# Kernel tuning notes

Hardware: AMD Instinct MI355X
Metric: run time of the kernel (lower is better)

Reference implementation:

```python
import jax, jax.numpy as jnp
import numpy as np

EPS = 1e-12  # matches tf l2_normalize epsilon behavior closely enough for testing

def setup_inputs() -> dict:
    key = jax.random.key(0)
    k1, k2 = jax.random.split(key)
    B, M, D = 512, 65536, 512
    context = jax.random.normal(k1, (B, D), dtype=jnp.float32)
    memory = jax.random.normal(k2, (M, D), dtype=jnp.float32)
    return {"context": context, "memory": memory}

def reference(context, memory):
    # tf.keras.losses.cosine_similarity returns NEGATIVE cosine similarity:
    # sim[b,m] = -sum(l2norm(context[b]) * l2norm(memory[m]))
    ctx_n = context / jnp.sqrt(jnp.maximum(jnp.sum(context * context, axis=-1, keepdims=True), EPS))
    mem_n = memory / jnp.sqrt(jnp.maximum(jnp.sum(memory * memory, axis=-1, keepdims=True), EPS))
    sim = -jnp.einsum('bd,md->bm', ctx_n, mem_n)  # [B, M]
    best = jnp.argmin(sim, axis=-1)               # [B], = argmax cosine
    # recall: gather then expand_dims(axis=0) -> [1, B, D]
    return memory[best][None, :, :]
```

## Files before the change

### kernel.cpp

```cpp
#include <hip/hip_runtime.h>
#include <hip/hip_bf16.h>
#include <stdint.h>

#define D_DIM 512
#define B_CTX 512
#define M_MEM 65536
#define BM 128
#define BB 128
#define BK 32
#define GBK 32
#define NIT (D_DIM / GBK)
#define LDSPAD 40
#define DELTA_COS 2.5e-3f
#define LISTCAP 2048
#define CVT_MEM_BLOCKS (M_MEM / 32)
#define CVT_BLOCKS (CVT_MEM_BLOCKS + B_CTX / 32)

typedef __attribute__((ext_vector_type(8))) short short8;
typedef __attribute__((ext_vector_type(4))) float floatx4;

__device__ __forceinline__ uint32_t f32_order(float s) {
    uint32_t u = __float_as_uint(s);
    return (u & 0x80000000u) ? ~u : (u | 0x80000000u);
}
__device__ __forceinline__ float f32_unorder(uint32_t v) {
    uint32_t u = (v & 0x80000000u) ? (v & 0x7FFFFFFFu) : ~v;
    return __uint_as_float(u);
}
__device__ __forceinline__ uint32_t pack_bf16_rtn(float a, float b) {
    uint32_t ua = __float_as_uint(a) + 0x8000u;
    uint32_t ub = __float_as_uint(b) + 0x8000u;
    return (ua >> 16) | (ub & 0xFFFF0000u);
}

typedef const __attribute__((address_space(1))) void gv_t;
typedef __attribute__((address_space(3))) void lv_t;
__device__ __forceinline__ void gload_lds16(const uint16_t* g, uint16_t* l) {
    __builtin_amdgcn_global_load_lds((gv_t*)g, (lv_t*)l, 16, 0, 0);
}

__global__ void detect_init(const uint32_t* __restrict__ mem_raw,
                            uint32_t* __restrict__ flag) {
    __shared__ int cnt;
    if (threadIdx.x == 0) cnt = 0;
    __syncthreads();
    int s = 0;
    #pragma unroll
    for (int i = 0; i < 8; ++i) {
        uint32_t u = mem_raw[threadIdx.x * 8 + i];
        uint32_t e = (u >> 7) & 0xFFu;
        s += (e >= 96u && e <= 144u) ? 1 : 0;
    }
    atomicAdd(&cnt, s);
    __syncthreads();
    if (threadIdx.x == 0) *flag = (cnt > 256) ? 1u : 0u;
}

__global__ __launch_bounds__(256) void convert_scale(const void* __restrict__ ctxv,
                                                     const void* __restrict__ memv,
                                                     const uint32_t* __restrict__ flag,
                                                     uint16_t* __restrict__ mem_s,
                                                     uint16_t* __restrict__ ctx_b) {
    const bool isbf = (*flag != 0u);
    const int lane = threadIdx.x & 63;
    const int w = threadIdx.x >> 6;
    if (blockIdx.x < CVT_MEM_BLOCKS) {
        const int gw = blockIdx.x * 4 + w;
        #pragma unroll
        for (int i = 0; i < 8; ++i) {
            const int r = gw * 8 + i;
            float x[8];
            if (isbf) {
                uint4 v = *((const uint4*)((const uint16_t*)memv + (size_t)r * D_DIM) + lane);
                uint32_t ww[4] = {v.x, v.y, v.z, v.w};
                #pragma unroll
                for (int j = 0; j < 4; ++j) {
                    x[2 * j]     = __uint_as_float(ww[j] << 16);
                    x[2 * j + 1] = __uint_as_float(ww[j] & 0xFFFF0000u);
                }
            } else {
                const float4* p = (const float4*)((const float*)memv + (size_t)r * D_DIM) + lane * 2;
                float4 a = p[0], bq = p[1];
                x[0] = a.x; x[1] = a.y; x[2] = a.z; x[3] = a.w;
                x[4] = bq.x; x[5] = bq.y; x[6] = bq.z; x[7] = bq.w;
            }
            float nsq = 0.f;
            #pragma unroll
            for (int j = 0; j < 8; ++j) nsq = fmaf(x[j], x[j], nsq);
            #pragma unroll
            for (int o = 32; o; o >>= 1) nsq += __shfl_xor(nsq, o, 64);
            const float invn = rsqrtf(fmaxf(nsq, 1e-12f));
            uint4 ov;
            ov.x = pack_bf16_rtn(x[0] * invn, x[1] * invn);
            ov.y = pack_bf16_rtn(x[2] * invn, x[3] * invn);
            ov.z = pack_bf16_rtn(x[4] * invn, x[5] * invn);
            ov.w = pack_bf16_rtn(x[6] * invn, x[7] * invn);
            *((uint4*)(mem_s + (size_t)r * D_DIM) + lane) = ov;
        }
    } else {
        const int gw = (blockIdx.x - CVT_MEM_BLOCKS) * 4 + w;
        #pragma unroll
        for (int i = 0; i < 8; ++i) {
            const int r = gw * 8 + i;
            uint4 ov;
            if (isbf) {
                ov = *((const uint4*)((const uint16_t*)ctxv + (size_t)r * D_DIM) + lane);
            } else {
                const float4* p = (const float4*)((const float*)ctxv + (size_t)r * D_DIM) + lane * 2;
                float4 a = p[0], bq = p[1];
                ov.x = pack_bf16_rtn(a.x, a.y);
                ov.y = pack_bf16_rtn(a.z, a.w);
                ov.z = pack_bf16_rtn(bq.x, bq.y);
                ov.w = pack_bf16_rtn(bq.z, bq.w);
            }
            *((uint4*)(ctx_b + (size_t)r * D_DIM) + lane) = ov;
        }
    }
}

#define STAGE(buf, kofs)                                                          \
    do {                                                                          \
        gload_lds16(ga0 + (kofs), &at[buf][0][0] + (size_t)((w << 6)) * 8);       \
        gload_lds16(ga1 + (kofs), &at[buf][0][0] + (size_t)(256 + (w << 6)) * 8); \
        gload_lds16(gb0 + (kofs), &bt[buf][0][0] + (size_t)((w << 6)) * 8);       \
        gload_lds16(gb1 + (kofs), &bt[buf][0][0] + (size_t)(256 + (w << 6)) * 8); \
    } while (0)

__global__ __launch_bounds__(256, 4) void score_mfma(const uint16_t* __restrict__ A,
                                                     const uint16_t* __restrict__ Bc,
                                                     uint32_t* __restrict__ tmax,
                                                     int coarse) {
    __shared__ __align__(16) uint16_t at[2][BM][GBK];
    __shared__ __align__(16) uint16_t bt[2][BB][GBK];
    __shared__ uint32_t s_gbest[8][BB];

    const int h  = blockIdx.y * gridDim.x + blockIdx.x;
    const int v  = (h & 7) * 256 + (h >> 3);
    const int bxp = v & 3;
    const int byp = v >> 2;

    const int t    = threadIdx.x;
    const int b0   = bxp * BB;
    const int m0   = byp * BM;
    const int lane = t & 63;
    const int w    = t >> 6;
    const int wm   = w >> 1;
    const int wb   = w & 1;
    const int quad = lane >> 4;
    const int l15  = lane & 15;
    const int srow = t >> 2;
    const int scol_sw = (((t & 3) ^ ((t >> 3) & 3)) << 3);
    const int rc = ((quad ^ ((l15 >> 1) & 3)) << 3);

    const uint16_t* ga0 = A  + (size_t)(m0 + srow) * D_DIM + scol_sw;
    const uint16_t* ga1 = A  + (size_t)(m0 + srow + 64) * D_DIM + scol_sw;
    const uint16_t* gb0 = Bc + (size_t)(b0 + srow) * D_DIM + scol_sw;
    const uint16_t* gb1 = Bc + (size_t)(b0 + srow + 64) * D_DIM + scol_sw;

    floatx4 acc[4][4];
    #pragma unroll
    for (int i = 0; i < 4; ++i)
        #pragma unroll
        for (int j = 0; j < 4; ++j)
            acc[i][j] = (floatx4){0.f, 0.f, 0.f, 0.f};

    STAGE(0, 0);

    #pragma unroll
    for (int it = 0; it < NIT; ++it) {
        const int cur = it & 1;
        if (it < NIT - 1) STAGE(cur ^ 1, (it + 1) * GBK);
        if (it < NIT - 1) asm volatile("s_waitcnt vmcnt(4)" ::: "memory");
        else              asm volatile("s_waitcnt vmcnt(0)" ::: "memory");
        __builtin_amdgcn_sched_barrier(0);
        __builtin_amdgcn_s_barrier();
        __builtin_amdgcn_sched_barrier(0);

        short8 af[4], bg[4];
        #pragma unroll
        for (int i = 0; i < 4; ++i)
            af[i] = *(const short8*)&at[cur][wm * 64 + i * 16 + l15][rc];
        #pragma unroll
        for (int j = 0; j < 4; ++j)
            bg[j] = *(const short8*)&bt[cur][wb * 64 + j * 16 + l15][rc];
        #pragma unroll
        for (int i = 0; i < 4; ++i)
            #pragma unroll
            for (int j = 0; j < 4; ++j)
                acc[i][j] = __builtin_amdgcn_mfma_f32_16x16x32_bf16(af[i], bg[j], acc[i][j], 0, 0, 0);

        if (it < NIT - 1) {
            __builtin_amdgcn_sched_barrier(0);
            asm volatile("s_waitcnt lgkmcnt(0)" ::: "memory");
            __builtin_amdgcn_s_barrier();
            __builtin_amdgcn_sched_barrier(0);
        }
    }

    #pragma unroll
    for (int i = 0; i < 4; ++i)
        #pragma unroll
        for (int j = 0; j < 4; ++j) {
            uint32_t k = 0;
            #pragma unroll
            for (int r = 0; r < 4; ++r) {
                uint32_t kk = f32_order(acc[i][j][r]);
                k = kk > k ? kk : k;
            }
            uint32_t o1 = __shfl_xor(k, 16, 64); k = o1 > k ? o1 : k;
            uint32_t o2 = __shfl_xor(k, 32, 64); k = o2 > k ? o2 : k;
            if (quad == 0) s_gbest[wm * 4 + i][wb * 64 + j * 16 + l15] = k;
        }
    __syncthreads();

    if (!coarse) {
        const int G0 = byp * 8;
        for (int e = t; e < 8 * BB; e += 256) {
            const int col = e >> 3, g = e & 7;
            tmax[(size_t)(b0 + col) * 4096 + G0 + g] = s_gbest[g][col];
        }
    } else {
        if (t < BB) {
            uint32_t k = s_gbest[0][t];
            #pragma unroll
            for (int g = 1; g < 8; ++g) k = s_gbest[g][t] > k ? s_gbest[g][t] : k;
            tmax[(size_t)(b0 + t) * 512 + byp] = k;
        }
    }
}

__global__ __launch_bounds__(256) void score_phase1(const void* __restrict__ ctxv,
                                                    const void* __restrict__ memv,
                                                    const uint32_t* __restrict__ flag,
                                                    uint32_t* __restrict__ tmax,
                                                    int coarse) {
    __shared__ __align__(16) uint16_t at[BM][LDSPAD];
    __shared__ __align__(16) uint16_t bt[BB][LDSPAD];
    __shared__ float s_nsq[BM];
    __shared__ uint32_t s_gbest[8][BB];

    const int t    = threadIdx.x;
    const int b0   = blockIdx.x * BB;
    const int m0   = blockIdx.y * BM;
    const int lane = t & 63;
    const int w    = t >> 6;
    const int wm   = w >> 1;
    const int wb   = w & 1;
    const int quad = lane >> 4;
    const int l15  = lane & 15;
    const int srow = t >> 2;
    const int scol = (t & 3) * 8;

    floatx4 acc[4][4];
    #pragma unroll
    for (int i = 0; i < 4; ++i)
        #pragma unroll
        for (int j = 0; j < 4; ++j)
            acc[i][j] = (floatx4){0.f, 0.f, 0.f, 0.f};

    float nsq0 = 0.f, nsq1 = 0.f;
    const bool isbf = (*flag != 0u);

    for (int k0 = 0; k0 < D_DIM; k0 += BK) {
        __syncthreads();
        if (isbf) {
            const uint16_t* mp = (const uint16_t*)memv;
            const uint16_t* cp = (const uint16_t*)ctxv;
            uint4 va0 = *(const uint4*)(mp + (size_t)(m0 + srow) * D_DIM + k0 + scol);
            uint4 va1 = *(const uint4*)(mp + (size_t)(m0 + srow + 64) * D_DIM + k0 + scol);
            uint4 vb0 = *(const uint4*)(cp + (size_t)(b0 + srow) * D_DIM + k0 + scol);
            uint4 vb1 = *(const uint4*)(cp + (size_t)(b0 + srow + 64) * D_DIM + k0 + scol);
            *(uint4*)&at[srow][scol] = va0;
            *(uint4*)&at[srow + 64][scol] = va1;
            *(uint4*)&bt[srow][scol] = vb0;
            *(uint4*)&bt[srow + 64][scol] = vb1;
            uint32_t wa0[4] = {va0.x, va0.y, va0.z, va0.w};
            uint32_t wa1[4] = {va1.x, va1.y, va1.z, va1.w};
            #pragma unroll
            for (int i = 0; i < 4; ++i) {
                float a = __uint_as_float(wa0[i] << 16);
                float b = __uint_as_float(wa0[i] & 0xFFFF0000u);
                nsq0 = fmaf(a, a, nsq0); nsq0 = fmaf(b, b, nsq0);
                float c = __uint_as_float(wa1[i] << 16);
                float d = __uint_as_float(wa1[i] & 0xFFFF0000u);
                nsq1 = fmaf(c, c, nsq1); nsq1 = fmaf(d, d, nsq1);
            }
        } else {
            const float* mp = (const float*)memv;
            const float* cp = (const float*)ctxv;
            const float4* pa0 = (const float4*)(mp + (size_t)(m0 + srow) * D_DIM + k0 + scol);
            const float4* pa1 = (const float4*)(mp + (size_t)(m0 + srow + 64) * D_DIM + k0 + scol);
            const float4* pb0 = (const float4*)(cp + (size_t)(b0 + srow) * D_DIM + k0 + scol);
            const float4* pb1 = (const float4*)(cp + (size_t)(b0 + srow + 64) * D_DIM + k0 + scol);
            float4 a0 = pa0[0], a1 = pa0[1], a2 = pa1[0], a3 = pa1[1];
            float4 c0 = pb0[0], c1 = pb0[1], c2 = pb1[0], c3 = pb1[1];
            uint4 va0 = {pack_bf16_rtn(a0.x, a0.y), pack_bf16_rtn(a0.z, a0.w),
                         pack_bf16_rtn(a1.x, a1.y), pack_bf16_rtn(a1.z, a1.w)};
            uint4 va1 = {pack_bf16_rtn(a2.x, a2.y), pack_bf16_rtn(a2.z, a2.w),
                         pack_bf16_rtn(a3.x, a3.y), pack_bf16_rtn(a3.z, a3.w)};
            uint4 vb0 = {pack_bf16_rtn(c0.x, c0.y), pack_bf16_rtn(c0.z, c0.w),
                         pack_bf16_rtn(c1.x, c1.y), pack_bf16_rtn(c1.z, c1.w)};
            uint4 vb1 = {pack_bf16_rtn(c2.x, c2.y), pack_bf16_rtn(c2.z, c2.w),
                         pack_bf16_rtn(c3.x, c3.y), pack_bf16_rtn(c3.z, c3.w)};
            *(uint4*)&at[srow][scol] = va0;
            *(uint4*)&at[srow + 64][scol] = va1;
            *(uint4*)&bt[srow][scol] = vb0;
            *(uint4*)&bt[srow + 64][scol] = vb1;
            nsq0 = fmaf(a0.x, a0.x, nsq0); nsq0 = fmaf(a0.y, a0.y, nsq0);
            nsq0 = fmaf(a0.z, a0.z, nsq0); nsq0 = fmaf(a0.w, a0.w, nsq0);
            nsq0 = fmaf(a1.x, a1.x, nsq0); nsq0 = fmaf(a1.y, a1.y, nsq0);
            nsq0 = fmaf(a1.z, a1.z, nsq0); nsq0 = fmaf(a1.w, a1.w, nsq0);
            nsq1 = fmaf(a2.x, a2.x, nsq1); nsq1 = fmaf(a2.y, a2.y, nsq1);
            nsq1 = fmaf(a2.z, a2.z, nsq1); nsq1 = fmaf(a2.w, a2.w, nsq1);
            nsq1 = fmaf(a3.x, a3.x, nsq1); nsq1 = fmaf(a3.y, a3.y, nsq1);
            nsq1 = fmaf(a3.z, a3.z, nsq1); nsq1 = fmaf(a3.w, a3.w, nsq1);
        }
        __syncthreads();

        short8 af[4], bg[4];
        #pragma unroll
        for (int i = 0; i < 4; ++i)
            af[i] = *(const short8*)&at[wm * 64 + i * 16 + l15][quad * 8];
        #pragma unroll
        for (int j = 0; j < 4; ++j)
            bg[j] = *(const short8*)&bt[wb * 64 + j * 16 + l15][quad * 8];

        #pragma unroll
        for (int i = 0; i < 4; ++i)
            #pragma unroll
            for (int j = 0; j < 4; ++j)
                acc[i][j] = __builtin_amdgcn_mfma_f32_16x16x32_bf16(af[i], bg[j], acc[i][j], 0, 0, 0);
    }

    nsq0 += __shfl_xor(nsq0, 1, 64); nsq0 += __shfl_xor(nsq0, 2, 64);
    nsq1 += __shfl_xor(nsq1, 1, 64); nsq1 += __shfl_xor(nsq1, 2, 64);
    __syncthreads();
    if ((t & 3) == 0) { s_nsq[srow] = nsq0; s_nsq[srow + 64] = nsq1; }
    __syncthreads();

    float invn[4][4];
    #pragma unroll
    for (int i = 0; i < 4; ++i)
        #pragma unroll
        for (int r = 0; r < 4; ++r)
            invn[i][r] = rsqrtf(fmaxf(s_nsq[wm * 64 + i * 16 + quad * 4 + r], 1e-12f));

    #pragma unroll
    for (int i = 0; i < 4; ++i)
        #pragma unroll
        for (int j = 0; j < 4; ++j) {
            uint32_t k = 0;
            #pragma unroll
            for (int r = 0; r < 4; ++r) {
                uint32_t kk = f32_order(acc[i][j][r] * invn[i][r]);
                k = kk > k ? kk : k;
            }
            uint32_t o1 = __shfl_xor(k, 16, 64); k = o1 > k ? o1 : k;
            uint32_t o2 = __shfl_xor(k, 32, 64); k = o2 > k ? o2 : k;
            if (quad == 0) s_gbest[wm * 4 + i][wb * 64 + j * 16 + l15] = k;
        }
    __syncthreads();

    if (!coarse) {
        const int G0 = blockIdx.y * 8;
        for (int e = t; e < 8 * BB; e += 256) {
            const int col = e >> 3, g = e & 7;
            tmax[(size_t)(b0 + col) * 4096 + G0 + g] = s_gbest[g][col];
        }
    } else {
        if (t < BB) {
            uint32_t k = s_gbest[0][t];
            #pragma unroll
            for (int g = 1; g < 8; ++g) k = s_gbest[g][t] > k ? s_gbest[g][t] : k;
            tmax[(size_t)(b0 + t) * 512 + blockIdx.y] = k;
        }
    }
}

__global__ __launch_bounds__(256) void phase2(const void* __restrict__ ctxv,
                                              const void* __restrict__ memv,
                                              const uint32_t* __restrict__ flag,
                                              const uint32_t* __restrict__ tmax,
                                              void* __restrict__ outv,
                                              int ngrp, int gshift) {
    __shared__ float s_ctx[D_DIM];
    __shared__ int s_list[LISTCAP];
    __shared__ int s_cnt;
    __shared__ uint32_t s_red[4];
    __shared__ float s_cn[4];
    __shared__ double s_d[4], s_n[4];
    __shared__ int s_m[4];
    __shared__ int s_bestm;

    const int b = blockIdx.x;
    const int t = threadIdx.x;
    const int lane = t & 63;
    const int w = t >> 6;
    const bool isbf = (*flag != 0u);
    const int gmask = (1 << gshift) - 1;

    if (t == 0) s_cnt = 0;
    if (isbf) {
        if (t < 64) {
            uint4 v = *((const uint4*)((const uint16_t*)ctxv + (size_t)b * D_DIM) + t);
            uint32_t ww[4] = {v.x, v.y, v.z, v.w};
            #pragma unroll
            for (int i = 0; i < 4; ++i) {
                s_ctx[t * 8 + 2 * i]     = __uint_as_float(ww[i] << 16);
                s_ctx[t * 8 + 2 * i + 1] = __uint_as_float(ww[i] & 0xFFFF0000u);
            }
        }
    } else {
        if (t < 128)
            ((float4*)s_ctx)[t] = ((const float4*)((const float*)ctxv + (size_t)b * D_DIM))[t];
    }
    __syncthreads();

    float cs = s_ctx[t] * s_ctx[t] + s_ctx[t + 256] * s_ctx[t + 256];
    #pragma unroll
    for (int o = 32; o; o >>= 1) cs += __shfl_xor(cs, o, 64);
    if (lane == 0) s_cn[w] = cs;

    const uint32_t* tk = tmax + (size_t)b * ngrp;
    const int nk = ngrp >> 8;
    uint32_t km = 0;
    for (int i = 0; i < nk; ++i) {
        uint32_t v = tk[t + (i << 8)];
        km = v > km ? v : km;
    }
    #pragma unroll
    for (int o = 32; o; o >>= 1) { uint32_t ot = __shfl_xor(km, o, 64); km = ot > km ? ot : km; }
    if (lane == 0) s_red[w] = km;
    __syncthreads();
    uint32_t kbest = s_red[0];
    #pragma unroll
    for (int i = 1; i < 4; ++i) kbest = s_red[i] > kbest ? s_red[i] : kbest;
    const float cnorm = sqrtf(s_cn[0] + s_cn[1] + s_cn[2] + s_cn[3]);
    const uint32_t keyT = f32_order(f32_unorder(kbest) - DELTA_COS * cnorm);

    for (int i = 0; i < nk; ++i) {
        uint32_t v = tk[t + (i << 8)];
        if (v >= keyT) {
            int idx = atomicAdd(&s_cnt, 1);
            if (idx < LISTCAP) s_list[idx] = t + (i << 8);
        }
    }
    __syncthreads();
    int cnt = s_cnt; if (cnt > LISTCAP) cnt = LISTCAP;
    const int total = cnt << gshift;

    double bd = -1.0e300, bn = 1.0;
    double bp = bd * 1.0e300;
    int bm = 0x7FFFFFFF;
    const float* cb = s_ctx + lane * 8;

    for (int base = w * 2; base < total; base += 8) {
        const bool has1 = (base + 1 < total);
        const int ia = base, ib = has1 ? base + 1 : base;
        const int ma = (s_list[ia >> gshift] << gshift) + (ia & gmask);
        const int mb = (s_list[ib >> gshift] << gshift) + (ib & gmask);
        double d0 = 0.0, n0 = 0.0, d1 = 0.0, n1 = 0.0;
        if (isbf) {
            uint4 va = *((const uint4*)((const uint16_t*)memv + (size_t)ma * D_DIM) + lane);
            uint4 vb = *((const uint4*)((const uint16_t*)memv + (size_t)mb * D_DIM) + lane);
            uint32_t wa[4] = {va.x, va.y, va.z, va.w};
            uint32_t wbv[4] = {vb.x, vb.y, vb.z, vb.w};
            #pragma unroll
            for (int i = 0; i < 4; ++i) {
                float a0 = __uint_as_float(wa[i] << 16);
                float a1 = __uint_as_float(wa[i] & 0xFFFF0000u);
                d0 += (double)a0 * (double)cb[2 * i];
                d0 += (double)a1 * (double)cb[2 * i + 1];
                n0 += (double)a0 * (double)a0 + (double)a1 * (double)a1;
                float b0v = __uint_as_float(wbv[i] << 16);
                float b1v = __uint_as_float(wbv[i] & 0xFFFF0000u);
                d1 += (double)b0v * (double)cb[2 * i];
                d1 += (double)b1v * (double)cb[2 * i + 1];
                n1 += (double)b0v * (double)b0v + (double)b1v * (double)b1v;
            }
        } else {
            const float4* pa = (const float4*)((const float*)memv + (size_t)ma * D_DIM) + lane * 2;
            const float4* pb = (const float4*)((const float*)memv + (size_t)mb * D_DIM) + lane * 2;
            float4 a0 = pa[0], a1 = pa[1], b0v = pb[0], b1v = pb[1];
            float xa[8] = {a0.x, a0.y, a0.z, a0.w, a1.x, a1.y, a1.z, a1.w};
            float xb[8] = {b0v.x, b0v.y, b0v.z, b0v.w, b1v.x, b1v.y, b1v.z, b1v.w};
            #pragma unroll
            for (int i = 0; i < 8; ++i) {
                d0 += (double)xa[i] * (double)cb[i];
                n0 += (double)xa[i] * (double)xa[i];
                d1 += (double)xb[i] * (double)cb[i];
                n1 += (double)xb[i] * (double)xb[i];
            }
        }
        #pragma unroll
        for (int o = 32; o; o >>= 1) {
            d0 += __shfl_xor(d0, o, 64);
            n0 += __shfl_xor(n0, o, 64);
            d1 += __shfl_xor(d1, o, 64);
            n1 += __shfl_xor(n1, o, 64);
        }
        double p0 = d0 * fabs(d0);
        double lhs = p0 * bn, rhs = bp * n0;
        if (lhs > rhs || (lhs == rhs && ma < bm)) { bd = d0; bn = n0; bp = p0; bm = ma; }
        if (has1) {
            double p1 = d1 * fabs(d1);
            double lhs1 = p1 * bn, rhs1 = bp * n1;
            if (lhs1 > rhs1 || (lhs1 == rhs1 && mb < bm)) { bd = d1; bn = n1; bp = p1; bm = mb; }
        }
    }
    if (lane == 0) { s_d[w] = bd; s_n[w] = bn; s_m[w] = bm; }
    __syncthreads();
    if (t == 0) {
        double cd = s_d[0], cn2 = s_n[0], cp = cd * fabs(cd);
        int cm = s_m[0];
        #pragma unroll
        for (int i = 1; i < 4; ++i) {
            double pd = s_d[i], pn = s_n[i], pp = pd * fabs(pd);
            double lhs = pp * cn2, rhs = cp * pn;
            if (lhs > rhs || (lhs == rhs && s_m[i] < cm)) { cd = pd; cn2 = pn; cp = pp; cm = s_m[i]; }
        }
        s_bestm = cm;
    }
    __syncthreads();
    const int mbest = s_bestm;
    if (isbf) {
        if (t < 64)
            ((uint4*)((uint16_t*)outv + (size_t)b * D_DIM))[t] =
                ((const uint4*)((const uint16_t*)memv + (size_t)mbest * D_DIM))[t];
    } else {
        if (t < 128)
            ((float4*)((float*)outv + (size_t)b * D_DIM))[t] =
                ((const float4*)((const float*)memv + (size_t)mbest * D_DIM))[t];
    }
}

extern "C" void kernel_launch(void* const* d_in, const int* in_sizes, int n_in,
                              void* d_out, int out_size, void* d_ws, size_t ws_size,
                              hipStream_t stream) {
    const void* ctx = d_in[0];
    const void* mem = d_in[1];
    if (in_sizes[0] > in_sizes[1]) { ctx = d_in[1]; mem = d_in[0]; }

    const size_t fineBytes   = (size_t)B_CTX * 4096 * 4;
    const size_t coarseBytes = (size_t)B_CTX * 512 * 4;
    const size_t ctxBytes    = (size_t)B_CTX * D_DIM * 2;
    const size_t memBytes    = (size_t)M_MEM * D_DIM * 2;
    const size_t fastBytes   = fineBytes + 256 + ctxBytes + memBytes;
    dim3 grid(B_CTX / BB, M_MEM / BM);

    if (ws_size >= fastBytes) {
        uint32_t* tmax  = (uint32_t*)d_ws;
        uint32_t* flag  = (uint32_t*)((char*)d_ws + fineBytes);
        uint16_t* ctx_b = (uint16_t*)((char*)d_ws + fineBytes + 256);
        uint16_t* mem_s = (uint16_t*)((char*)d_ws + fineBytes + 256 + ctxBytes);
        detect_init<<<1, 64, 0, stream>>>((const uint32_t*)mem, flag);
        convert_scale<<<CVT_BLOCKS, 256, 0, stream>>>(ctx, mem, flag, mem_s, ctx_b);
        score_mfma<<<grid, 256, 0, stream>>>(mem_s, ctx_b, tmax, 0);
        phase2<<<B_CTX, 256, 0, stream>>>(ctx, mem, flag, tmax, d_out, 4096, 4);
    } else if (ws_size >= fineBytes + 256) {
        uint32_t* tmax = (uint32_t*)d_ws;
        uint32_t* flag = (uint32_t*)((char*)d_ws + fineBytes);
        detect_init<<<1, 64, 0, stream>>>((const uint32_t*)mem, flag);
        score_phase1<<<grid, 256, 0, stream>>>(ctx, mem, flag, tmax, 0);
        phase2<<<B_CTX, 256, 0, stream>>>(ctx, mem, flag, tmax, d_out, 4096, 4);
    } else {
        uint32_t* tmax = (uint32_t*)d_ws;
        uint32_t* flag = (uint32_t*)((char*)d_ws + coarseBytes);
        detect_init<<<1, 64, 0, stream>>>((const uint32_t*)mem, flag);
        score_phase1<<<grid, 256, 0, stream>>>(ctx, mem, flag, tmax, 1);
        phase2<<<B_CTX, 256, 0, stream>>>(ctx, mem, flag, tmax, d_out, 512, 7);
    }
}
```

Before: 272.6 us.

## Widen score_mfma block tile to 128x256 with 512 threads

The MFMA scoring kernel now covers 256 context columns per block instead of 128, using 8 waves (2x4) in a 512-thread block. The grid halves along the context dimension, so each staged memory tile is reused across twice as many context rows, which lowers global and LDS traffic for the large memory operand. In exchange the block uses more LDS and threads, which may reduce the number of resident blocks per CU, and the swizzled block ordering and staging wait counts are adjusted to match.

```diff
diff --git a/kernel.cpp b/kernel.cpp
--- a/kernel.cpp
+++ b/kernel.cpp
@@ -7,6 +7,7 @@
 #define M_MEM 65536
 #define BM 128
 #define BB 128
+#define BBW 256
 #define BK 32
 #define GBK 32
 #define NIT (D_DIM / GBK)
@@ -118,44 +119,41 @@
     }
 }
 
-#define STAGE(buf, kofs)                                                          \
-    do {                                                                          \
-        gload_lds16(ga0 + (kofs), &at[buf][0][0] + (size_t)((w << 6)) * 8);       \
-        gload_lds16(ga1 + (kofs), &at[buf][0][0] + (size_t)(256 + (w << 6)) * 8); \
-        gload_lds16(gb0 + (kofs), &bt[buf][0][0] + (size_t)((w << 6)) * 8);       \
-        gload_lds16(gb1 + (kofs), &bt[buf][0][0] + (size_t)(256 + (w << 6)) * 8); \
+#define STAGE2(buf, kofs)                                                          \
+    do {                                                                           \
+        gload_lds16(ga  + (kofs), &at[buf][0][0] + (size_t)((w << 6)) * 8);        \
+        gload_lds16(gb0 + (kofs), &bt[buf][0][0] + (size_t)((w << 6)) * 8);        \
+        gload_lds16(gb1 + (kofs), &bt[buf][0][0] + (size_t)(512 + (w << 6)) * 8);  \
     } while (0)
 
-__global__ __launch_bounds__(256, 4) void score_mfma(const uint16_t* __restrict__ A,
+__global__ __launch_bounds__(512, 4) void score_mfma(const uint16_t* __restrict__ A,
                                                      const uint16_t* __restrict__ Bc,
                                                      uint32_t* __restrict__ tmax,
                                                      int coarse) {
     __shared__ __align__(16) uint16_t at[2][BM][GBK];
-    __shared__ __align__(16) uint16_t bt[2][BB][GBK];
-    __shared__ uint32_t s_gbest[8][BB];
+    __shared__ __align__(16) uint16_t bt[2][BBW][GBK];
+    __shared__ uint32_t s_gbest[8][BBW];
 
     const int h  = blockIdx.y * gridDim.x + blockIdx.x;
-    const int v  = (h & 7) * 256 + (h >> 3);
-    const int bxp = v & 3;
-    const int byp = v >> 2;
+    const int v  = (h & 7) * 128 + (h >> 3);
+    const int bxp = v & 1;
+    const int byp = v >> 1;
 
     const int t    = threadIdx.x;
-    const int b0   = bxp * BB;
+    const int b0   = bxp * BBW;
     const int m0   = byp * BM;
     const int lane = t & 63;
     const int w    = t >> 6;
-    const int wm   = w >> 1;
-    const int wb   = w & 1;
+    const int wm   = w >> 2;
+    const int wb   = w & 3;
     const int quad = lane >> 4;
     const int l15  = lane & 15;
-    const int srow = t >> 2;
     const int scol_sw = (((t & 3) ^ ((t >> 3) & 3)) << 3);
     const int rc = ((quad ^ ((l15 >> 1) & 3)) << 3);
 
-    const uint16_t* ga0 = A  + (size_t)(m0 + srow) * D_DIM + scol_sw;
-    const uint16_t* ga1 = A  + (size_t)(m0 + srow + 64) * D_DIM + scol_sw;
-    const uint16_t* gb0 = Bc + (size_t)(b0 + srow) * D_DIM + scol_sw;
-    const uint16_t* gb1 = Bc + (size_t)(b0 + srow + 64) * D_DIM + scol_sw;
+    const uint16_t* ga  = A  + (size_t)(m0 + (t >> 2)) * D_DIM + scol_sw;
+    const uint16_t* gb0 = Bc + (size_t)(b0 + (t >> 2)) * D_DIM + scol_sw;
+    const uint16_t* gb1 = gb0 + (size_t)128 * D_DIM;
 
     floatx4 acc[4][4];
     #pragma unroll
@@ -164,13 +162,13 @@
         for (int j = 0; j < 4; ++j)
             acc[i][j] = (floatx4){0.f, 0.f, 0.f, 0.f};
 
-    STAGE(0, 0);
+    STAGE2(0, 0);
 
     #pragma unroll
     for (int it = 0; it < NIT; ++it) {
         const int cur = it & 1;
-        if (it < NIT - 1) STAGE(cur ^ 1, (it + 1) * GBK);
-        if (it < NIT - 1) asm volatile("s_waitcnt vmcnt(4)" ::: "memory");
+        if (it < NIT - 1) STAGE2(cur ^ 1, (it + 1) * GBK);
+        if (it < NIT - 1) asm volatile("s_waitcnt vmcnt(3)" ::: "memory");
         else              asm volatile("s_waitcnt vmcnt(0)" ::: "memory");
         __builtin_amdgcn_sched_barrier(0);
         __builtin_amdgcn_s_barrier();
@@ -215,12 +213,12 @@
 
     if (!coarse) {
         const int G0 = byp * 8;
-        for (int e = t; e < 8 * BB; e += 256) {
+        for (int e = t; e < 8 * BBW; e += 512) {
             const int col = e >> 3, g = e & 7;
             tmax[(size_t)(b0 + col) * 4096 + G0 + g] = s_gbest[g][col];
         }
     } else {
-        if (t < BB) {
+        if (t < BBW) {
             uint32_t k = s_gbest[0][t];
             #pragma unroll
             for (int g = 1; g < 8; ++g) k = s_gbest[g][t] > k ? s_gbest[g][t] : k;
@@ -546,26 +544,28 @@
     const size_t ctxBytes    = (size_t)B_CTX * D_DIM * 2;
     const size_t memBytes    = (size_t)M_MEM * D_DIM * 2;
     const size_t fastBytes   = fineBytes + 256 + ctxBytes + memBytes;
-    dim3 grid(B_CTX / BB, M_MEM / BM);
 
     if (ws_size >= fastBytes) {
         uint32_t* tmax  = (uint32_t*)d_ws;
         uint32_t* flag  = (uint32_t*)((char*)d_ws + fineBytes);
         uint16_t* ctx_b = (uint16_t*)((char*)d_ws + fineBytes + 256);
         uint16_t* mem_s = (uint16_t*)((char*)d_ws + fineBytes + 256 + ctxBytes);
+        dim3 grid(B_CTX / BBW, M_MEM / BM);
         detect_init<<<1, 64, 0, stream>>>((const uint32_t*)mem, flag);
         convert_scale<<<CVT_BLOCKS, 256, 0, stream>>>(ctx, mem, flag, mem_s, ctx_b);
-        score_mfma<<<grid, 256, 0, stream>>>(mem_s, ctx_b, tmax, 0);
+        score_mfma<<<grid, 512, 0, stream>>>(mem_s, ctx_b, tmax, 0);
         phase2<<<B_CTX, 256, 0, stream>>>(ctx, mem, flag, tmax, d_out, 4096, 4);
     } else if (ws_size >= fineBytes + 256) {
         uint32_t* tmax = (uint32_t*)d_ws;
         uint32_t* flag = (uint32_t*)((char*)d_ws + fineBytes);
+        dim3 grid(B_CTX / BB, M_MEM / BM);
         detect_init<<<1, 64, 0, stream>>>((const uint32_t*)mem, flag);
         score_phase1<<<grid, 256, 0, stream>>>(ctx, mem, flag, tmax, 0);
         phase2<<<B_CTX, 256, 0, stream>>>(ctx, mem, flag, tmax, d_out, 4096, 4);
     } else {
         uint32_t* tmax = (uint32_t*)d_ws;
         uint32_t* flag = (uint32_t*)((char*)d_ws + coarseBytes);
+        dim3 grid(B_CTX / BB, M_MEM / BM);
         detect_init<<<1, 64, 0, stream>>>((const uint32_t*)mem, flag);
         score_phase1<<<grid, 256, 0, stream>>>(ctx, mem, flag, tmax, 1);
         phase2<<<B_CTX, 256, 0, stream>>>(ctx, mem, flag, tmax, d_out, 512, 7);
```

Measured after the change: 270.5 us. Within noise of the previous version (-0.8%).
